# Optimization experiments

Hardware: AMD Instinct MI355X
Metric: run time of the kernel (lower is better)

Reference implementation:

```python
import jax, jax.numpy as jnp
import numpy as np

N_NODES = 100000
N_EDGES = 1600000
HID = 128
BOND = 16
BN_EPS = 1e-5


def setup_inputs() -> dict:
    key = jax.random.key(0)
    ks = jax.random.split(key, 12)
    sb = 1.0 / np.sqrt(BOND)
    sh = 1.0 / np.sqrt(HID)
    return {
        "features": jax.random.normal(ks[0], (N_NODES, HID), jnp.float32),
        "edge_feats": jax.random.normal(ks[1], (N_EDGES, BOND), jnp.float32),
        "src": jax.random.randint(ks[2], (N_EDGES,), 0, N_NODES, jnp.int32),
        "dst": jax.random.randint(ks[3], (N_EDGES,), 0, N_NODES, jnp.int32),
        "Wb": jax.random.uniform(ks[4], (HID, BOND), jnp.float32, -sb, sb),
        "bb": jax.random.uniform(ks[5], (HID,), jnp.float32, -sb, sb),
        "W1": jax.random.uniform(ks[6], (HID, HID), jnp.float32, -sh, sh),
        "b1": jax.random.uniform(ks[7], (HID,), jnp.float32, -sh, sh),
        "W2": jax.random.uniform(ks[8], (HID, HID), jnp.float32, -sh, sh),
        "b2": jax.random.uniform(ks[9], (HID,), jnp.float32, -sh, sh),
        "gamma1": jnp.ones((HID,), jnp.float32),
        "beta1": jnp.zeros((HID,), jnp.float32),
        "gamma2": jnp.ones((HID,), jnp.float32),
        "beta2": jnp.zeros((HID,), jnp.float32),
    }


def _batchnorm(x, gamma, beta):
    # BatchNorm1d in training mode: normalize with batch stats (biased var).
    mean = jnp.mean(x, axis=0)
    var = jnp.var(x, axis=0)
    return (x - mean) * jax.lax.rsqrt(var + BN_EPS) * gamma + beta


def reference(features, edge_feats, src, dst, Wb, bb, W1, b1, W2, b2,
              gamma1, beta1, gamma2, beta2):
    n = features.shape[0]
    # edge linear: [E, BOND] -> [E, HID]
    eh = edge_feats @ Wb.T + bb
    # mailbox sums: sum of src node features and edge messages per dst node
    h1 = jax.ops.segment_sum(features[src], dst, num_segments=n)  # [N, HID]
    h2 = jax.ops.segment_sum(eh, dst, num_segments=n)             # [N, HID]
    h = jax.nn.relu(_batchnorm(h1 @ W1.T + b1 + h2, gamma1, beta1))
    h = jax.nn.relu(_batchnorm(h @ W2.T + b2 + features, gamma2, beta2))
    return h
```

## Files before the change

kernel.cpp:

```cpp
#include <hip/hip_runtime.h>

#define NN 100000
#define NE 1600000
#define HID 128
#define KEXT 160
#define ROWB 320
#define BSH 9
#define BNODES 512
#define NB 196
#define P2B 256
#define EPB2 6250
#define T2 2048
#define SCAP 10240
#define BN_EPS 1e-5f

typedef __attribute__((ext_vector_type(8))) short bf16x8;
typedef __attribute__((ext_vector_type(4))) float f32x4;

__device__ inline unsigned short f2bf(float x) {
  union { float f; unsigned u; } v; v.f = x;
  unsigned r = v.u + 0x7FFFu + ((v.u >> 16) & 1u);
  return (unsigned short)(r >> 16);
}
__device__ inline unsigned pk2(float a, float b) {
  return (unsigned)f2bf(a) | ((unsigned)f2bf(b) << 16);
}
__device__ inline float bflo(unsigned p) { return __uint_as_float(p << 16); }
__device__ inline float bfhi(unsigned p) { return __uint_as_float(p & 0xffff0000u); }

__device__ inline void gload_lds16(const void* g, void* l) {
  __builtin_amdgcn_global_load_lds((const __attribute__((address_space(1))) void*)g,
                                   (__attribute__((address_space(3))) void*)l, 16, 0, 0);
}

__global__ __launch_bounds__(256) void fbw_k(const float* __restrict__ f,
                                             unsigned* __restrict__ fb,
                                             const float* __restrict__ W1,
                                             const float* __restrict__ Wb,
                                             const float* __restrict__ bb,
                                             const float* __restrict__ b1,
                                             const float* __restrict__ W2,
                                             unsigned short* __restrict__ W1e,
                                             unsigned short* __restrict__ W2e,
                                             const int* __restrict__ dst,
                                             int* __restrict__ cnts_s) {
  __shared__ int bh[NB];
  if (blockIdx.x < 25000) {
    int i = blockIdx.x * 256 + threadIdx.x;
    float2 v = ((const float2*)f)[i];
    fb[i] = pk2(v.x, v.y);
  } else if (blockIdx.x < 25080) {
    int idx = (blockIdx.x - 25000) * 256 + threadIdx.x;
    if (idx < 128 * KEXT) {
      int c = idx / KEXT, k = idx - c * KEXT;
      float v1 = 0.f;
      if (k < 128) v1 = W1[c * HID + k];
      else if (k < 144) v1 = Wb[c * 16 + (k - 128)];
      else if (k == 144) v1 = bb[c];
      else if (k == 145) v1 = b1[c];
      W1e[idx] = f2bf(v1);
    }
    if (idx < 128 * 128) W2e[idx] = f2bf(W2[(idx >> 7) * HID + (idx & 127)]);
  } else {
    int blk = blockIdx.x - 25080;
    int b0 = blk * EPB2, e1 = b0 + EPB2;
    for (int i = threadIdx.x; i < NB; i += 256) bh[i] = 0;
    __syncthreads();
    for (int e = b0 + threadIdx.x; e < e1; e += 256) atomicAdd(&bh[dst[e] >> BSH], 1);
    __syncthreads();
    for (int i = threadIdx.x; i < NB; i += 256) cnts_s[i * P2B + blk] = bh[i];
  }
}

__global__ __launch_bounds__(P2B) void cscan_k(int* __restrict__ cnts_s,
                                               int* __restrict__ bcnt_s,
                                               int* __restrict__ bcnt_r) {
  __shared__ int s[P2B];
  int b = blockIdx.x, t = threadIdx.x;
  int x = cnts_s[b * P2B + t];
  int xs = (x + 7) & ~7;
  s[t] = xs; __syncthreads();
  for (int off = 1; off < P2B; off <<= 1) {
    int v = (t >= off) ? s[t - off] : 0; __syncthreads();
    s[t] += v; __syncthreads();
  }
  cnts_s[b * P2B + t] = s[t] - xs;
  if (t == P2B - 1) bcnt_s[b] = s[t];
  __syncthreads();
  s[t] = x; __syncthreads();
  for (int off = 1; off < P2B; off <<= 1) {
    int v = (t >= off) ? s[t - off] : 0; __syncthreads();
    s[t] += v; __syncthreads();
  }
  if (t == P2B - 1) bcnt_r[b] = s[t];
}

__global__ __launch_bounds__(256) void bscan_k(const int* __restrict__ bcnt_r,
                                               const int* __restrict__ bcnt_s,
                                               int* __restrict__ bbase_r,
                                               int* __restrict__ bbase_s,
                                               int* __restrict__ rs) {
  __shared__ int s[256];
  int t = threadIdx.x;
#pragma unroll
  for (int pass = 0; pass < 2; ++pass) {
    const int* in = (pass == 0) ? bcnt_r : bcnt_s;
    int* out = (pass == 0) ? bbase_r : bbase_s;
    int x = (t < NB) ? in[t] : 0;
    s[t] = x; __syncthreads();
    for (int off = 1; off < 256; off <<= 1) {
      int v = (t >= off) ? s[t - off] : 0; __syncthreads();
      s[t] += v; __syncthreads();
    }
    if (t < NB) out[t] = s[t] - x;
    if (t == NB - 1) out[NB] = s[t];
    __syncthreads();
  }
  if (t == 0) rs[NN] = NE;
}

__global__ __launch_bounds__(1024) void part3_k(const int* __restrict__ src,
                                                const int* __restrict__ dst,
                                                const float* __restrict__ ef,
                                                const int* __restrict__ bbase_s,
                                                const int* __restrict__ cnts_s,
                                                unsigned* __restrict__ stg,
                                                float4* __restrict__ efb) {
  __shared__ int th[NB], ts[NB], cnt2[NB], run[NB], st_s[NB];
  __shared__ int sscan[256];
  __shared__ unsigned spk[T2];
  __shared__ float4 eflds[T2 * 2];
  int blk = blockIdx.x, tid = threadIdx.x;
  int b0 = blk * EPB2, e1 = b0 + EPB2;
  for (int i = tid; i < NB; i += 1024) {
    run[i] = 0;
    st_s[i] = bbase_s[i] + cnts_s[i * P2B + blk];
  }
  for (int t0 = b0; t0 < e1; t0 += T2) {
    int tc = min(T2, e1 - t0);
    for (int i = tid; i < NB; i += 1024) { th[i] = 0; cnt2[i] = 0; }
    __syncthreads();
    for (int le = tid; le < tc; le += 1024) {
      int e = t0 + le;
      atomicAdd(&th[dst[e] >> BSH], 1);
      const float4* efp = (const float4*)(ef + (size_t)e * 16);
      float4 e0 = efp[0], e1v = efp[1], e2 = efp[2], e3 = efp[3];
      float4 w0, w1;
      w0.x = __uint_as_float(pk2(e0.x, e0.y));  w0.y = __uint_as_float(pk2(e0.z, e0.w));
      w0.z = __uint_as_float(pk2(e1v.x, e1v.y)); w0.w = __uint_as_float(pk2(e1v.z, e1v.w));
      w1.x = __uint_as_float(pk2(e2.x, e2.y));  w1.y = __uint_as_float(pk2(e2.z, e2.w));
      w1.z = __uint_as_float(pk2(e3.x, e3.y));  w1.w = __uint_as_float(pk2(e3.z, e3.w));
      eflds[le * 2] = w0;
      eflds[le * 2 + 1] = w1;
    }
    __syncthreads();
    if (tid < 256) sscan[tid] = (tid < NB) ? th[tid] : 0;
    __syncthreads();
    for (int off = 1; off < 256; off <<= 1) {
      int v = 0;
      if (tid < 256 && tid >= off) v = sscan[tid - off];
      __syncthreads();
      if (tid < 256) sscan[tid] += v;
      __syncthreads();
    }
    if (tid < NB) ts[tid] = sscan[tid] - th[tid];
    __syncthreads();
    for (int le = tid; le < tc; le += 1024) {
      int b = dst[t0 + le] >> BSH;
      int slot = ts[b] + atomicAdd(&cnt2[b], 1);
      spk[slot] = ((unsigned)b << 11) | (unsigned)le;
    }
    __syncthreads();
    for (int s2 = tid; s2 < tc; s2 += 1024) {
      unsigned pk = spk[s2];
      int b = pk >> 11, le = pk & 2047;
      int e = t0 + le;
      int gs = st_s[b] + run[b] + (s2 - ts[b]);
      int d9 = dst[e] & (BNODES - 1);
      stg[gs] = (unsigned)src[e] | ((unsigned)d9 << 17) | (1u << 26);
      efb[(size_t)gs * 2] = eflds[le * 2];
      efb[(size_t)gs * 2 + 1] = eflds[le * 2 + 1];
    }
    __syncthreads();
    for (int i = tid; i < NB; i += 1024) run[i] += th[i];
    __syncthreads();
  }
  for (int i = tid; i < NB; i += 1024) {
    int c = run[i];
    int cs = (c + 7) & ~7;
    for (int j = c; j < cs; ++j) stg[st_s[i] + j] = 0u;
  }
}

__global__ __launch_bounds__(512) void bsort_k(const unsigned* __restrict__ stg,
                                               const int* __restrict__ bbase_s,
                                               const int* __restrict__ bbase_r,
                                               const unsigned* __restrict__ efbu,
                                               int* __restrict__ rs,
                                               unsigned* __restrict__ fin,
                                               unsigned* __restrict__ efsum) {
  __shared__ int h[BNODES], sc[BNODES], cur[BNODES];
  __shared__ int tot;
  __shared__ unsigned slds[SCAP];
  int b = blockIdx.x, n0 = b << BSH, tid = threadIdx.x;
  int s0p = bbase_s[b], e1p = bbase_s[b + 1];
  int s0r = bbase_r[b];
  h[tid] = 0;
  __syncthreads();
  for (int i = s0p + tid; i < e1p; i += 512) {
    unsigned rec = stg[i];
    if (rec >> 26) atomicAdd(&h[(rec >> 17) & (BNODES - 1)], 1);
  }
  __syncthreads();
  sc[tid] = h[tid];
  __syncthreads();
  for (int off = 1; off < BNODES; off <<= 1) {
    int v = (tid >= off) ? sc[tid - off] : 0;
    __syncthreads();
    sc[tid] += v;
    __syncthreads();
  }
  int excl = sc[tid] - h[tid];
  cur[tid] = excl;
  int n = n0 + tid;
  if (n < NN) rs[n] = s0r + excl;
  if (tid == BNODES - 1) tot = sc[tid];
  __syncthreads();
  for (int i = s0p + tid; i < e1p; i += 512) {
    unsigned rec = stg[i];
    if (rec >> 26) {
      int d = (rec >> 17) & (BNODES - 1);
      int p = atomicAdd(&cur[d], 1);
      slds[p] = (rec & 0x1FFFF) | ((unsigned)(i - s0p) << 17);
    }
  }
  __syncthreads();
  int T = tot;
  for (int j = tid; j < T; j += 512) fin[s0r + j] = slds[j] & 0x1FFFF;
  if (n < NN) {
    float a[16];
#pragma unroll
    for (int k = 0; k < 16; ++k) a[k] = 0.f;
    for (int j = excl; j < sc[tid]; ++j) {
      unsigned rec = slds[j];
      const unsigned* ep = efbu + ((size_t)s0p + (rec >> 17)) * 8;
#pragma unroll
      for (int k = 0; k < 8; ++k) {
        unsigned u = ep[k];
        a[2 * k] += bflo(u);
        a[2 * k + 1] += bfhi(u);
      }
    }
    unsigned* op = efsum + (size_t)n * 8;
#pragma unroll
    for (int k = 0; k < 8; ++k) op[k] = pk2(a[2 * k], a[2 * k + 1]);
  }
}

__global__ __launch_bounds__(256) void feg_k(const unsigned* __restrict__ fb,
                                             const int* __restrict__ rs,
                                             const unsigned* __restrict__ fin,
                                             const unsigned* __restrict__ efsum,
                                             unsigned short* __restrict__ A1) {
  int bid = (int)(blockIdx.x & 7) * 3125 + (int)(blockIdx.x >> 3);
  int wid = threadIdx.x >> 6, lane = threadIdx.x & 63;
  int node = bid * 4 + wid;
  if (node >= NN) return;
  int start = rs[node], end = rs[node + 1];
  float ax0 = 0.f, ay0 = 0.f, ax1 = 0.f, ay1 = 0.f;
  float ax2 = 0.f, ay2 = 0.f, ax3 = 0.f, ay3 = 0.f;
  float ax4 = 0.f, ay4 = 0.f, ax5 = 0.f, ay5 = 0.f;
  float ax6 = 0.f, ay6 = 0.f, ax7 = 0.f, ay7 = 0.f;
  int i = start;
  for (; i + 8 <= end; i += 8) {
    int sl = 0;
    if (lane < 8) sl = (int)fin[i + lane];
    int s0 = __shfl(sl, 0), s1 = __shfl(sl, 1), s2 = __shfl(sl, 2), s3 = __shfl(sl, 3);
    int s4 = __shfl(sl, 4), s5 = __shfl(sl, 5), s6 = __shfl(sl, 6), s7 = __shfl(sl, 7);
    unsigned p0 = fb[s0 * 64 + lane];
    unsigned p1 = fb[s1 * 64 + lane];
    unsigned p2 = fb[s2 * 64 + lane];
    unsigned p3 = fb[s3 * 64 + lane];
    unsigned p4 = fb[s4 * 64 + lane];
    unsigned p5 = fb[s5 * 64 + lane];
    unsigned p6 = fb[s6 * 64 + lane];
    unsigned p7 = fb[s7 * 64 + lane];
    ax0 += bflo(p0); ay0 += bfhi(p0);
    ax1 += bflo(p1); ay1 += bfhi(p1);
    ax2 += bflo(p2); ay2 += bfhi(p2);
    ax3 += bflo(p3); ay3 += bfhi(p3);
    ax4 += bflo(p4); ay4 += bfhi(p4);
    ax5 += bflo(p5); ay5 += bfhi(p5);
    ax6 += bflo(p6); ay6 += bfhi(p6);
    ax7 += bflo(p7); ay7 += bfhi(p7);
  }
  for (; i < end; ++i) {
    int sl = 0;
    if (lane == 0) sl = (int)fin[i];
    int s0 = __shfl(sl, 0);
    unsigned p0 = fb[s0 * 64 + lane];
    ax0 += bflo(p0); ay0 += bfhi(p0);
  }
  float ax = ((ax0 + ax1) + (ax2 + ax3)) + ((ax4 + ax5) + (ax6 + ax7));
  float ay = ((ay0 + ay1) + (ay2 + ay3)) + ((ay4 + ay5) + (ay6 + ay7));
  char* rowp = (char*)A1 + (size_t)node * ROWB;
  *(unsigned*)(rowp + lane * 4) = pk2(ax, ay);
  if (lane < 8) {
    *(unsigned*)(rowp + 256 + 4 * lane) = efsum[(size_t)node * 8 + lane];
  } else if (lane < 16) {
    int j2 = lane - 8;
    *(unsigned*)(rowp + 288 + 4 * j2) =
        (j2 == 0) ? pk2((float)(end - start), 1.0f) : 0u;
  }
}

__global__ __launch_bounds__(256) void gemm1_k(
    const unsigned short* __restrict__ A, const unsigned short* __restrict__ W,
    unsigned short* __restrict__ outb, float* __restrict__ ssum, float* __restrict__ ssq) {
  __shared__ __align__(16) char sA[64 * ROWB];
  __shared__ __align__(16) char sW[128 * ROWB];
  const int tid = threadIdx.x;
  const int wid = tid >> 6, lane = tid & 63;
  const size_t r0 = (size_t)blockIdx.x * 64;

#pragma unroll
  for (int q = 0; q < 5; ++q) {
    int s = q * 256 + tid;
    int row = (s * 3277) >> 16;
    int c = s - row * 20;
    int csrc = (c < 16) ? (c ^ (row & 7)) : (16 + ((c - 16) ^ (row & 3)));
    gload_lds16((const char*)A + (r0 + row) * ROWB + csrc * 16,
                sA + (size_t)(q * 256 + wid * 64) * 16);
  }
#pragma unroll
  for (int q = 0; q < 10; ++q) {
    int s = q * 256 + tid;
    int row = (s * 3277) >> 16;
    int c = s - row * 20;
    int csrc = (c < 16) ? (c ^ (row & 7)) : (16 + ((c - 16) ^ (row & 3)));
    gload_lds16((const char*)W + (size_t)row * ROWB + csrc * 16,
                sW + (size_t)(q * 256 + wid * 64) * 16);
  }
  __syncthreads();

  const int l15 = lane & 15;
  const int kgr = lane >> 4;
  const int arow = wid * 16 + l15;
  bf16x8 afrag[5];
#pragma unroll
  for (int ks = 0; ks < 5; ++ks) {
    int creq = ks * 4 + kgr;
    int csw = (creq < 16) ? (creq ^ (arow & 7)) : (16 + ((creq - 16) ^ (arow & 3)));
    afrag[ks] = *(const bf16x8*)(sA + arow * ROWB + csw * 16);
  }
  f32x4 acc[8];
#pragma unroll
  for (int ct = 0; ct < 8; ++ct) acc[ct] = (f32x4){0.f, 0.f, 0.f, 0.f};
#pragma unroll
  for (int ct = 0; ct < 8; ++ct) {
    int brow = ct * 16 + l15;
#pragma unroll
    for (int ks = 0; ks < 5; ++ks) {
      int creq = ks * 4 + kgr;
      int csw = (creq < 16) ? (creq ^ (brow & 7)) : (16 + ((creq - 16) ^ (brow & 3)));
      bf16x8 bfrag = *(const bf16x8*)(sW + brow * ROWB + csw * 16);
      acc[ct] = __builtin_amdgcn_mfma_f32_16x16x32_bf16(afrag[ks], bfrag, acc[ct], 0, 0, 0);
    }
  }

  const size_t orow0 = r0 + wid * 16 + kgr * 4;
  float cs[8], cq[8];
#pragma unroll
  for (int ct = 0; ct < 8; ++ct) {
    int col = ct * 16 + l15;
    float s_ = 0.f, q_ = 0.f;
#pragma unroll
    for (int r = 0; r < 4; ++r) {
      size_t row = orow0 + r;
      if (row < NN) {
        float v = acc[ct][r];
        outb[row * HID + col] = f2bf(v);
        s_ += v; q_ += v * v;
      }
    }
    cs[ct] = s_; cq[ct] = q_;
  }
#pragma unroll
  for (int ct = 0; ct < 8; ++ct) {
    cs[ct] += __shfl_xor(cs[ct], 16); cs[ct] += __shfl_xor(cs[ct], 32);
    cq[ct] += __shfl_xor(cq[ct], 16); cq[ct] += __shfl_xor(cq[ct], 32);
  }
  __syncthreads();
  float* red = (float*)sA;
  if (lane < 16) {
#pragma unroll
    for (int ct = 0; ct < 8; ++ct) {
      red[wid * 256 + ct * 16 + l15] = cs[ct];
      red[wid * 256 + 128 + ct * 16 + l15] = cq[ct];
    }
  }
  __syncthreads();
  if (tid < 128) {
    float s_ = red[tid] + red[256 + tid] + red[512 + tid] + red[768 + tid];
    float q_ = red[128 + tid] + red[384 + tid] + red[640 + tid] + red[896 + tid];
    atomicAdd(&ssum[tid], s_);
    atomicAdd(&ssq[tid], q_);
  }
}

__global__ __launch_bounds__(256) void gemm2_k(
    const unsigned* __restrict__ t, const unsigned short* __restrict__ W,
    const float* __restrict__ ssum, const float* __restrict__ ssq,
    const float* __restrict__ gamma, const float* __restrict__ beta,
    const float* __restrict__ b2, const float* __restrict__ F,
    unsigned short* __restrict__ outb, float* __restrict__ ssum2,
    float* __restrict__ ssq2) {
  __shared__ __align__(16) char sA[64 * 256];
  __shared__ __align__(16) char sW[128 * 256];
  __shared__ float ssc[128], ssh[128];
  const int tid = threadIdx.x;
  const int wid = tid >> 6, lane = tid & 63;
  const size_t r0 = (size_t)blockIdx.x * 64;

  if (tid < 128) {
    const float invN = 1.f / (float)NN;
    float m = ssum[tid] * invN;
    float var = ssq[tid] * invN - m * m;
    float inv = rsqrtf(var + BN_EPS);
    float sc = gamma[tid] * inv;
    ssc[tid] = sc;
    ssh[tid] = beta[tid] - m * sc;
  }
#pragma unroll
  for (int q = 0; q < 8; ++q) {
    int s = q * 256 + tid;
    int row = s >> 4, c = s & 15;
    int csrc = c ^ (row & 7);
    gload_lds16((const char*)W + (size_t)row * 256 + csrc * 16,
                sW + (size_t)(q * 256 + wid * 64) * 16);
  }
  __syncthreads();

  {
    int sr = tid >> 2;
    int c0 = (tid & 3) * 4;
    size_t grow = r0 + sr;
    bool valid = grow < NN;
    const unsigned* trow = t + grow * 64;
#pragma unroll
    for (int cc = 0; cc < 4; ++cc) {
      int c = c0 + cc;
      unsigned o0 = 0, o1 = 0, o2 = 0, o3 = 0;
      if (valid) {
        unsigned p0 = trow[c * 4 + 0], p1 = trow[c * 4 + 1];
        unsigned p2 = trow[c * 4 + 2], p3 = trow[c * 4 + 3];
        int k = c * 8;
        o0 = pk2(fmaxf(0.f, fmaf(bflo(p0), ssc[k + 0], ssh[k + 0])),
                 fmaxf(0.f, fmaf(bfhi(p0), ssc[k + 1], ssh[k + 1])));
        o1 = pk2(fmaxf(0.f, fmaf(bflo(p1), ssc[k + 2], ssh[k + 2])),
                 fmaxf(0.f, fmaf(bfhi(p1), ssc[k + 3], ssh[k + 3])));
        o2 = pk2(fmaxf(0.f, fmaf(bflo(p2), ssc[k + 4], ssh[k + 4])),
                 fmaxf(0.f, fmaf(bfhi(p2), ssc[k + 5], ssh[k + 5])));
        o3 = pk2(fmaxf(0.f, fmaf(bflo(p3), ssc[k + 6], ssh[k + 6])),
                 fmaxf(0.f, fmaf(bfhi(p3), ssc[k + 7], ssh[k + 7])));
      }
      int csw = c ^ (sr & 7);
      uint4 w4; w4.x = o0; w4.y = o1; w4.z = o2; w4.w = o3;
      *(uint4*)(sA + sr * 256 + csw * 16) = w4;
    }
  }
  __syncthreads();

  const int l15 = lane & 15;
  const int kgr = lane >> 4;
  const int arow = wid * 16 + l15;
  bf16x8 afrag[4];
#pragma unroll
  for (int ks = 0; ks < 4; ++ks) {
    int creq = ks * 4 + kgr;
    int csw = creq ^ (arow & 7);
    afrag[ks] = *(const bf16x8*)(sA + arow * 256 + csw * 16);
  }
  f32x4 acc[8];
#pragma unroll
  for (int ct = 0; ct < 8; ++ct) acc[ct] = (f32x4){0.f, 0.f, 0.f, 0.f};
#pragma unroll
  for (int ct = 0; ct < 8; ++ct) {
    int brow = ct * 16 + l15;
#pragma unroll
    for (int ks = 0; ks < 4; ++ks) {
      int creq = ks * 4 + kgr;
      int csw = creq ^ (brow & 7);
      bf16x8 bfrag = *(const bf16x8*)(sW + brow * 256 + csw * 16);
      acc[ct] = __builtin_amdgcn_mfma_f32_16x16x32_bf16(afrag[ks], bfrag, acc[ct], 0, 0, 0);
    }
  }

  const size_t orow0 = r0 + wid * 16 + kgr * 4;
  float cs[8], cq[8];
#pragma unroll
  for (int ct = 0; ct < 8; ++ct) {
    int col = ct * 16 + l15;
    float b2v = b2[col];
    float s_ = 0.f, q_ = 0.f;
#pragma unroll
    for (int r = 0; r < 4; ++r) {
      size_t row = orow0 + r;
      if (row < NN) {
        float v = acc[ct][r] + b2v + F[row * HID + col];
        outb[row * HID + col] = f2bf(v);
        s_ += v; q_ += v * v;
      }
    }
    cs[ct] = s_; cq[ct] = q_;
  }
#pragma unroll
  for (int ct = 0; ct < 8; ++ct) {
    cs[ct] += __shfl_xor(cs[ct], 16); cs[ct] += __shfl_xor(cs[ct], 32);
    cq[ct] += __shfl_xor(cq[ct], 16); cq[ct] += __shfl_xor(cq[ct], 32);
  }
  __syncthreads();
  float* red = (float*)sA;
  if (lane < 16) {
#pragma unroll
    for (int ct = 0; ct < 8; ++ct) {
      red[wid * 256 + ct * 16 + l15] = cs[ct];
      red[wid * 256 + 128 + ct * 16 + l15] = cq[ct];
    }
  }
  __syncthreads();
  if (tid < 128) {
    float s_ = red[tid] + red[256 + tid] + red[512 + tid] + red[768 + tid];
    float q_ = red[128 + tid] + red[384 + tid] + red[640 + tid] + red[896 + tid];
    atomicAdd(&ssum2[tid], s_);
    atomicAdd(&ssq2[tid], q_);
  }
}

__global__ __launch_bounds__(256) void bn_final_k(const unsigned* __restrict__ t,
                                                  const float* __restrict__ ssum,
                                                  const float* __restrict__ ssq,
                                                  const float* __restrict__ gamma,
                                                  const float* __restrict__ beta,
                                                  float* __restrict__ o) {
  __shared__ float ssc[128], ssh[128];
  int tid = threadIdx.x;
  if (tid < 128) {
    const float invN = 1.f / (float)NN;
    float m = ssum[tid] * invN;
    float var = ssq[tid] * invN - m * m;
    float inv = rsqrtf(var + BN_EPS);
    float sc = gamma[tid] * inv;
    ssc[tid] = sc;
    ssh[tid] = beta[tid] - m * sc;
  }
  __syncthreads();
  int i = blockIdx.x * 256 + tid;
  if (i >= NN * 64) return;
  unsigned p = t[i];
  int c = (i & 63) * 2;
  float2 v;
  v.x = fmaxf(0.f, fmaf(bflo(p), ssc[c], ssh[c]));
  v.y = fmaxf(0.f, fmaf(bfhi(p), ssc[c + 1], ssh[c + 1]));
  ((float2*)o)[i] = v;
}

extern "C" void kernel_launch(void* const* d_in, const int* in_sizes, int n_in,
                              void* d_out, int out_size, void* d_ws, size_t ws_size,
                              hipStream_t stream) {
  (void)in_sizes; (void)n_in; (void)out_size; (void)ws_size;
  const float* features   = (const float*)d_in[0];
  const float* edge_feats = (const float*)d_in[1];
  const int*   src        = (const int*)d_in[2];
  const int*   dst        = (const int*)d_in[3];
  const float* Wb         = (const float*)d_in[4];
  const float* bb         = (const float*)d_in[5];
  const float* W1         = (const float*)d_in[6];
  const float* b1         = (const float*)d_in[7];
  const float* W2         = (const float*)d_in[8];
  const float* b2         = (const float*)d_in[9];
  const float* gamma1     = (const float*)d_in[10];
  const float* beta1      = (const float*)d_in[11];
  const float* gamma2     = (const float*)d_in[12];
  const float* beta2      = (const float*)d_in[13];
  float* outp = (float*)d_out;

  char* wsb = (char*)d_ws;
  size_t off = 0;
  auto alloc = [&](size_t nbytes) -> void* {
    off = (off + 255) & ~(size_t)255;
    void* p = wsb + off;
    off += nbytes;
    return p;
  };
  const size_t STGN = (size_t)NE + 7 * NB * P2B + 64;
  int* row_start = (int*)alloc((size_t)(NN + 1) * 4);
  int* bcnt_r    = (int*)alloc(NB * 4);
  int* bcnt_s    = (int*)alloc(NB * 4);
  int* bbase_r   = (int*)alloc((NB + 1) * 4);
  int* bbase_s   = (int*)alloc((NB + 1) * 4);
  int* cnts_s    = (int*)alloc((size_t)NB * P2B * 4);
  float* stats   = (float*)alloc(512 * 4);
  unsigned* featb = (unsigned*)alloc((size_t)NN * 64 * 4);
  unsigned short* A1e = (unsigned short*)alloc((size_t)100032 * ROWB);
  unsigned short* W1e = (unsigned short*)alloc(128 * KEXT * 2);
  unsigned short* W2e = (unsigned short*)alloc(128 * 128 * 2);
  unsigned* stg  = (unsigned*)alloc(STGN * 4);
  unsigned* fin  = (unsigned*)alloc((size_t)NE * 4);
  float4* efb    = (float4*)alloc(STGN * 32);
  unsigned* efsum = (unsigned*)alloc((size_t)NN * 32);
  unsigned short* tbuf = (unsigned short*)featb;

  hipMemsetAsync(stats, 0, 512 * 4, stream);
  hipMemsetAsync((char*)A1e + (size_t)NN * ROWB, 0, 32 * ROWB, stream);

  fbw_k<<<25336, 256, 0, stream>>>(features, featb, W1, Wb, bb, b1, W2, W1e, W2e,
                                   dst, cnts_s);
  cscan_k<<<NB, P2B, 0, stream>>>(cnts_s, bcnt_s, bcnt_r);
  bscan_k<<<1, 256, 0, stream>>>(bcnt_r, bcnt_s, bbase_r, bbase_s, row_start);
  part3_k<<<P2B, 1024, 0, stream>>>(src, dst, edge_feats, bbase_s, cnts_s, stg, efb);
  bsort_k<<<NB, 512, 0, stream>>>(stg, bbase_s, bbase_r, (const unsigned*)efb,
                                  row_start, fin, efsum);
  feg_k<<<25000, 256, 0, stream>>>(featb, row_start, fin, efsum, A1e);

  gemm1_k<<<1563, 256, 0, stream>>>(A1e, W1e, tbuf, stats, stats + 128);
  gemm2_k<<<1563, 256, 0, stream>>>((const unsigned*)tbuf, W2e, stats, stats + 128,
                                    gamma1, beta1, b2, features, tbuf,
                                    stats + 256, stats + 384);
  bn_final_k<<<25000, 256, 0, stream>>>((const unsigned*)tbuf, stats + 256, stats + 384,
                                        gamma2, beta2, outp);
}
```

Measured before the change: 333.0 us.

## Double GEMM row tiles to 128 and shard BN stat atomics across 16 slots

Both GEMM kernels now process 128 rows per block, using two 16-row MFMA tiles per wave that share each B fragment load, and the grid is halved. BatchNorm statistics are accumulated into 16 partial slots indexed by block to reduce atomic contention. Small single-block kernels reduce those slots and precompute scale/shift, so the per-block BN setup in gemm2 and bn_final is removed. gemm2's A staging now uses vectorized uint4 loads, and the padded buffers are zeroed so the larger tiles can read past NN safely. In exchange there are two extra tiny launches and more LDS and registers per block, which may lower occupancy.

Result: faster. 304.1 us (-8.7%).

```diff
diff --git a/kernel.cpp b/kernel.cpp
--- a/kernel.cpp
+++ b/kernel.cpp
@@ -12,6 +12,8 @@
 #define EPB2 6250
 #define T2 2048
 #define SCAP 10240
+#define NROWP 100096
+#define GGRID 782
 #define BN_EPS 1e-5f
 
 typedef __attribute__((ext_vector_type(8))) short bf16x8;
@@ -316,15 +318,15 @@
 
 __global__ __launch_bounds__(256) void gemm1_k(
     const unsigned short* __restrict__ A, const unsigned short* __restrict__ W,
-    unsigned short* __restrict__ outb, float* __restrict__ ssum, float* __restrict__ ssq) {
-  __shared__ __align__(16) char sA[64 * ROWB];
+    unsigned short* __restrict__ outb, float* __restrict__ statsP) {
+  __shared__ __align__(16) char sA[128 * ROWB];
   __shared__ __align__(16) char sW[128 * ROWB];
   const int tid = threadIdx.x;
   const int wid = tid >> 6, lane = tid & 63;
-  const size_t r0 = (size_t)blockIdx.x * 64;
-
-#pragma unroll
-  for (int q = 0; q < 5; ++q) {
+  const size_t r0 = (size_t)blockIdx.x * 128;
+
+#pragma unroll
+  for (int q = 0; q < 10; ++q) {
     int s = q * 256 + tid;
     int row = (s * 3277) >> 16;
     int c = s - row * 20;
@@ -345,17 +347,22 @@
 
   const int l15 = lane & 15;
   const int kgr = lane >> 4;
-  const int arow = wid * 16 + l15;
-  bf16x8 afrag[5];
-#pragma unroll
-  for (int ks = 0; ks < 5; ++ks) {
-    int creq = ks * 4 + kgr;
-    int csw = (creq < 16) ? (creq ^ (arow & 7)) : (16 + ((creq - 16) ^ (arow & 3)));
-    afrag[ks] = *(const bf16x8*)(sA + arow * ROWB + csw * 16);
-  }
-  f32x4 acc[8];
-#pragma unroll
-  for (int ct = 0; ct < 8; ++ct) acc[ct] = (f32x4){0.f, 0.f, 0.f, 0.f};
+  bf16x8 afrag[2][5];
+#pragma unroll
+  for (int rt = 0; rt < 2; ++rt) {
+    int arow = wid * 32 + rt * 16 + l15;
+#pragma unroll
+    for (int ks = 0; ks < 5; ++ks) {
+      int creq = ks * 4 + kgr;
+      int csw = (creq < 16) ? (creq ^ (arow & 7)) : (16 + ((creq - 16) ^ (arow & 3)));
+      afrag[rt][ks] = *(const bf16x8*)(sA + arow * ROWB + csw * 16);
+    }
+  }
+  f32x4 acc[2][8];
+#pragma unroll
+  for (int rt = 0; rt < 2; ++rt)
+#pragma unroll
+    for (int ct = 0; ct < 8; ++ct) acc[rt][ct] = (f32x4){0.f, 0.f, 0.f, 0.f};
 #pragma unroll
   for (int ct = 0; ct < 8; ++ct) {
     int brow = ct * 16 + l15;
@@ -364,26 +371,30 @@
       int creq = ks * 4 + kgr;
       int csw = (creq < 16) ? (creq ^ (brow & 7)) : (16 + ((creq - 16) ^ (brow & 3)));
       bf16x8 bfrag = *(const bf16x8*)(sW + brow * ROWB + csw * 16);
-      acc[ct] = __builtin_amdgcn_mfma_f32_16x16x32_bf16(afrag[ks], bfrag, acc[ct], 0, 0, 0);
-    }
-  }
-
-  const size_t orow0 = r0 + wid * 16 + kgr * 4;
+      acc[0][ct] = __builtin_amdgcn_mfma_f32_16x16x32_bf16(afrag[0][ks], bfrag, acc[0][ct], 0, 0, 0);
+      acc[1][ct] = __builtin_amdgcn_mfma_f32_16x16x32_bf16(afrag[1][ks], bfrag, acc[1][ct], 0, 0, 0);
+    }
+  }
+
   float cs[8], cq[8];
 #pragma unroll
-  for (int ct = 0; ct < 8; ++ct) {
-    int col = ct * 16 + l15;
-    float s_ = 0.f, q_ = 0.f;
-#pragma unroll
-    for (int r = 0; r < 4; ++r) {
-      size_t row = orow0 + r;
-      if (row < NN) {
-        float v = acc[ct][r];
-        outb[row * HID + col] = f2bf(v);
-        s_ += v; q_ += v * v;
+  for (int ct = 0; ct < 8; ++ct) { cs[ct] = 0.f; cq[ct] = 0.f; }
+#pragma unroll
+  for (int rt = 0; rt < 2; ++rt) {
+    const size_t orow0 = r0 + wid * 32 + rt * 16 + kgr * 4;
+#pragma unroll
+    for (int ct = 0; ct < 8; ++ct) {
+      int col = ct * 16 + l15;
+#pragma unroll
+      for (int r = 0; r < 4; ++r) {
+        size_t row = orow0 + r;
+        if (row < NN) {
+          float v = acc[rt][ct][r];
+          outb[row * HID + col] = f2bf(v);
+          cs[ct] += v; cq[ct] += v * v;
+        }
       }
     }
-    cs[ct] = s_; cq[ct] = q_;
   }
 #pragma unroll
   for (int ct = 0; ct < 8; ++ct) {
@@ -400,36 +411,49 @@
     }
   }
   __syncthreads();
-  if (tid < 128) {
+  if (tid < 256) {
+    float* base = statsP + (size_t)(blockIdx.x & 15) * 512;
     float s_ = red[tid] + red[256 + tid] + red[512 + tid] + red[768 + tid];
-    float q_ = red[128 + tid] + red[384 + tid] + red[640 + tid] + red[896 + tid];
-    atomicAdd(&ssum[tid], s_);
-    atomicAdd(&ssq[tid], q_);
+    atomicAdd(&base[tid], s_);
+  }
+}
+
+__global__ void bnred_k(const float* __restrict__ statsP, int base,
+                        const float* __restrict__ gamma, const float* __restrict__ beta,
+                        float* __restrict__ scale, float* __restrict__ shift) {
+  int c = threadIdx.x;
+  if (c < 128) {
+    float s_ = 0.f, q_ = 0.f;
+#pragma unroll
+    for (int i = 0; i < 16; ++i) {
+      s_ += statsP[i * 512 + base + c];
+      q_ += statsP[i * 512 + base + 128 + c];
+    }
+    const float invN = 1.f / (float)NN;
+    float m = s_ * invN;
+    float var = q_ * invN - m * m;
+    float inv = rsqrtf(var + BN_EPS);
+    float sc = gamma[c] * inv;
+    scale[c] = sc;
+    shift[c] = beta[c] - m * sc;
   }
 }
 
 __global__ __launch_bounds__(256) void gemm2_k(
     const unsigned* __restrict__ t, const unsigned short* __restrict__ W,
-    const float* __restrict__ ssum, const float* __restrict__ ssq,
-    const float* __restrict__ gamma, const float* __restrict__ beta,
+    const float* __restrict__ scale, const float* __restrict__ shift,
     const float* __restrict__ b2, const float* __restrict__ F,
-    unsigned short* __restrict__ outb, float* __restrict__ ssum2,
-    float* __restrict__ ssq2) {
-  __shared__ __align__(16) char sA[64 * 256];
+    unsigned short* __restrict__ outb, float* __restrict__ statsP) {
+  __shared__ __align__(16) char sA[128 * 256];
   __shared__ __align__(16) char sW[128 * 256];
   __shared__ float ssc[128], ssh[128];
   const int tid = threadIdx.x;
   const int wid = tid >> 6, lane = tid & 63;
-  const size_t r0 = (size_t)blockIdx.x * 64;
+  const size_t r0 = (size_t)blockIdx.x * 128;
 
   if (tid < 128) {
-    const float invN = 1.f / (float)NN;
-    float m = ssum[tid] * invN;
-    float var = ssq[tid] * invN - m * m;
-    float inv = rsqrtf(var + BN_EPS);
-    float sc = gamma[tid] * inv;
-    ssc[tid] = sc;
-    ssh[tid] = beta[tid] - m * sc;
+    ssc[tid] = scale[tid];
+    ssh[tid] = shift[tid];
   }
 #pragma unroll
   for (int q = 0; q < 8; ++q) {
@@ -441,49 +465,46 @@
   }
   __syncthreads();
 
-  {
-    int sr = tid >> 2;
-    int c0 = (tid & 3) * 4;
+#pragma unroll
+  for (int q = 0; q < 8; ++q) {
+    int s = q * 256 + tid;
+    int sr = s >> 4, c = s & 15;
     size_t grow = r0 + sr;
-    bool valid = grow < NN;
-    const unsigned* trow = t + grow * 64;
-#pragma unroll
-    for (int cc = 0; cc < 4; ++cc) {
-      int c = c0 + cc;
-      unsigned o0 = 0, o1 = 0, o2 = 0, o3 = 0;
-      if (valid) {
-        unsigned p0 = trow[c * 4 + 0], p1 = trow[c * 4 + 1];
-        unsigned p2 = trow[c * 4 + 2], p3 = trow[c * 4 + 3];
-        int k = c * 8;
-        o0 = pk2(fmaxf(0.f, fmaf(bflo(p0), ssc[k + 0], ssh[k + 0])),
-                 fmaxf(0.f, fmaf(bfhi(p0), ssc[k + 1], ssh[k + 1])));
-        o1 = pk2(fmaxf(0.f, fmaf(bflo(p1), ssc[k + 2], ssh[k + 2])),
-                 fmaxf(0.f, fmaf(bfhi(p1), ssc[k + 3], ssh[k + 3])));
-        o2 = pk2(fmaxf(0.f, fmaf(bflo(p2), ssc[k + 4], ssh[k + 4])),
-                 fmaxf(0.f, fmaf(bfhi(p2), ssc[k + 5], ssh[k + 5])));
-        o3 = pk2(fmaxf(0.f, fmaf(bflo(p3), ssc[k + 6], ssh[k + 6])),
-                 fmaxf(0.f, fmaf(bfhi(p3), ssc[k + 7], ssh[k + 7])));
-      }
-      int csw = c ^ (sr & 7);
-      uint4 w4; w4.x = o0; w4.y = o1; w4.z = o2; w4.w = o3;
-      *(uint4*)(sA + sr * 256 + csw * 16) = w4;
-    }
+    uint4 v = make_uint4(0, 0, 0, 0);
+    if (grow < NN) v = *(const uint4*)(t + grow * 64 + c * 4);
+    int k = c * 8;
+    unsigned o0 = pk2(fmaxf(0.f, fmaf(bflo(v.x), ssc[k + 0], ssh[k + 0])),
+                      fmaxf(0.f, fmaf(bfhi(v.x), ssc[k + 1], ssh[k + 1])));
+    unsigned o1 = pk2(fmaxf(0.f, fmaf(bflo(v.y), ssc[k + 2], ssh[k + 2])),
+                      fmaxf(0.f, fmaf(bfhi(v.y), ssc[k + 3], ssh[k + 3])));
+    unsigned o2 = pk2(fmaxf(0.f, fmaf(bflo(v.z), ssc[k + 4], ssh[k + 4])),
+                      fmaxf(0.f, fmaf(bfhi(v.z), ssc[k + 5], ssh[k + 5])));
+    unsigned o3 = pk2(fmaxf(0.f, fmaf(bflo(v.w), ssc[k + 6], ssh[k + 6])),
+                      fmaxf(0.f, fmaf(bfhi(v.w), ssc[k + 7], ssh[k + 7])));
+    int csw = c ^ (sr & 7);
+    uint4 w4; w4.x = o0; w4.y = o1; w4.z = o2; w4.w = o3;
+    *(uint4*)(sA + sr * 256 + csw * 16) = w4;
   }
   __syncthreads();
 
   const int l15 = lane & 15;
   const int kgr = lane >> 4;
-  const int arow = wid * 16 + l15;
-  bf16x8 afrag[4];
-#pragma unroll
-  for (int ks = 0; ks < 4; ++ks) {
-    int creq = ks * 4 + kgr;
-    int csw = creq ^ (arow & 7);
-    afrag[ks] = *(const bf16x8*)(sA + arow * 256 + csw * 16);
-  }
-  f32x4 acc[8];
-#pragma unroll
-  for (int ct = 0; ct < 8; ++ct) acc[ct] = (f32x4){0.f, 0.f, 0.f, 0.f};
+  bf16x8 afrag[2][4];
+#pragma unroll
+  for (int rt = 0; rt < 2; ++rt) {
+    int arow = wid * 32 + rt * 16 + l15;
+#pragma unroll
+    for (int ks = 0; ks < 4; ++ks) {
+      int creq = ks * 4 + kgr;
+      int csw = creq ^ (arow & 7);
+      afrag[rt][ks] = *(const bf16x8*)(sA + arow * 256 + csw * 16);
+    }
+  }
+  f32x4 acc[2][8];
+#pragma unroll
+  for (int rt = 0; rt < 2; ++rt)
+#pragma unroll
+    for (int ct = 0; ct < 8; ++ct) acc[rt][ct] = (f32x4){0.f, 0.f, 0.f, 0.f};
 #pragma unroll
   for (int ct = 0; ct < 8; ++ct) {
     int brow = ct * 16 + l15;
@@ -492,27 +513,31 @@
       int creq = ks * 4 + kgr;
       int csw = creq ^ (brow & 7);
       bf16x8 bfrag = *(const bf16x8*)(sW + brow * 256 + csw * 16);
-      acc[ct] = __builtin_amdgcn_mfma_f32_16x16x32_bf16(afrag[ks], bfrag, acc[ct], 0, 0, 0);
-    }
-  }
-
-  const size_t orow0 = r0 + wid * 16 + kgr * 4;
+      acc[0][ct] = __builtin_amdgcn_mfma_f32_16x16x32_bf16(afrag[0][ks], bfrag, acc[0][ct], 0, 0, 0);
+      acc[1][ct] = __builtin_amdgcn_mfma_f32_16x16x32_bf16(afrag[1][ks], bfrag, acc[1][ct], 0, 0, 0);
+    }
+  }
+
   float cs[8], cq[8];
 #pragma unroll
-  for (int ct = 0; ct < 8; ++ct) {
-    int col = ct * 16 + l15;
-    float b2v = b2[col];
-    float s_ = 0.f, q_ = 0.f;
-#pragma unroll
-    for (int r = 0; r < 4; ++r) {
-      size_t row = orow0 + r;
-      if (row < NN) {
-        float v = acc[ct][r] + b2v + F[row * HID + col];
-        outb[row * HID + col] = f2bf(v);
-        s_ += v; q_ += v * v;
+  for (int ct = 0; ct < 8; ++ct) { cs[ct] = 0.f; cq[ct] = 0.f; }
+#pragma unroll
+  for (int rt = 0; rt < 2; ++rt) {
+    const size_t orow0 = r0 + wid * 32 + rt * 16 + kgr * 4;
+#pragma unroll
+    for (int ct = 0; ct < 8; ++ct) {
+      int col = ct * 16 + l15;
+      float b2v = b2[col];
+#pragma unroll
+      for (int r = 0; r < 4; ++r) {
+        size_t row = orow0 + r;
+        if (row < NN) {
+          float v = acc[rt][ct][r] + b2v + F[row * HID + col];
+          outb[row * HID + col] = f2bf(v);
+          cs[ct] += v; cq[ct] += v * v;
+        }
       }
     }
-    cs[ct] = s_; cq[ct] = q_;
   }
 #pragma unroll
   for (int ct = 0; ct < 8; ++ct) {
@@ -529,31 +554,20 @@
     }
   }
   __syncthreads();
-  if (tid < 128) {
+  if (tid < 256) {
+    float* base = statsP + (size_t)(blockIdx.x & 15) * 512 + 256;
     float s_ = red[tid] + red[256 + tid] + red[512 + tid] + red[768 + tid];
-    float q_ = red[128 + tid] + red[384 + tid] + red[640 + tid] + red[896 + tid];
-    atomicAdd(&ssum2[tid], s_);
-    atomicAdd(&ssq2[tid], q_);
+    atomicAdd(&base[tid], s_);
   }
 }
 
 __global__ __launch_bounds__(256) void bn_final_k(const unsigned* __restrict__ t,
-                                                  const float* __restrict__ ssum,
-                                                  const float* __restrict__ ssq,
-                                                  const float* __restrict__ gamma,
-                                                  const float* __restrict__ beta,
+                                                  const float* __restrict__ scale,
+                                                  const float* __restrict__ shift,
                                                   float* __restrict__ o) {
   __shared__ float ssc[128], ssh[128];
   int tid = threadIdx.x;
-  if (tid < 128) {
-    const float invN = 1.f / (float)NN;
-    float m = ssum[tid] * invN;
-    float var = ssq[tid] * invN - m * m;
-    float inv = rsqrtf(var + BN_EPS);
-    float sc = gamma[tid] * inv;
-    ssc[tid] = sc;
-    ssh[tid] = beta[tid] - m * sc;
-  }
+  if (tid < 128) { ssc[tid] = scale[tid]; ssh[tid] = shift[tid]; }
   __syncthreads();
   int i = blockIdx.x * 256 + tid;
   if (i >= NN * 64) return;
@@ -600,9 +614,10 @@
   int* bbase_r   = (int*)alloc((NB + 1) * 4);
   int* bbase_s   = (int*)alloc((NB + 1) * 4);
   int* cnts_s    = (int*)alloc((size_t)NB * P2B * 4);
-  float* stats   = (float*)alloc(512 * 4);
-  unsigned* featb = (unsigned*)alloc((size_t)NN * 64 * 4);
-  unsigned short* A1e = (unsigned short*)alloc((size_t)100032 * ROWB);
+  float* statsP  = (float*)alloc(16 * 512 * 4);
+  float* scsh    = (float*)alloc(512 * 4);
+  unsigned* featb = (unsigned*)alloc((size_t)NROWP * 64 * 4);
+  unsigned short* A1e = (unsigned short*)alloc((size_t)NROWP * ROWB);
   unsigned short* W1e = (unsigned short*)alloc(128 * KEXT * 2);
   unsigned short* W2e = (unsigned short*)alloc(128 * 128 * 2);
   unsigned* stg  = (unsigned*)alloc(STGN * 4);
@@ -611,8 +626,9 @@
   unsigned* efsum = (unsigned*)alloc((size_t)NN * 32);
   unsigned short* tbuf = (unsigned short*)featb;
 
-  hipMemsetAsync(stats, 0, 512 * 4, stream);
-  hipMemsetAsync((char*)A1e + (size_t)NN * ROWB, 0, 32 * ROWB, stream);
+  hipMemsetAsync(statsP, 0, 16 * 512 * 4, stream);
+  hipMemsetAsync((char*)A1e + (size_t)NN * ROWB, 0, (NROWP - NN) * ROWB, stream);
+  hipMemsetAsync((char*)featb + (size_t)NN * 256, 0, (NROWP - NN) * 256, stream);
 
   fbw_k<<<25336, 256, 0, stream>>>(features, featb, W1, Wb, bb, b1, W2, W1e, W2e,
                                    dst, cnts_s);
@@ -623,10 +639,11 @@
                                   row_start, fin, efsum);
   feg_k<<<25000, 256, 0, stream>>>(featb, row_start, fin, efsum, A1e);
 
-  gemm1_k<<<1563, 256, 0, stream>>>(A1e, W1e, tbuf, stats, stats + 128);
-  gemm2_k<<<1563, 256, 0, stream>>>((const unsigned*)tbuf, W2e, stats, stats + 128,
-                                    gamma1, beta1, b2, features, tbuf,
-                                    stats + 256, stats + 384);
-  bn_final_k<<<25000, 256, 0, stream>>>((const unsigned*)tbuf, stats + 256, stats + 384,
-                                        gamma2, beta2, outp);
-}
+  gemm1_k<<<GGRID, 256, 0, stream>>>(A1e, W1e, tbuf, statsP);
+  bnred_k<<<1, 128, 0, stream>>>(statsP, 0, gamma1, beta1, scsh, scsh + 128);
+  gemm2_k<<<GGRID, 256, 0, stream>>>((const unsigned*)tbuf, W2e, scsh, scsh + 128,
+                                     b2, features, tbuf, statsP);
+  bnred_k<<<1, 128, 0, stream>>>(statsP, 256, gamma2, beta2, scsh + 256, scsh + 384);
+  bn_final_k<<<25000, 256, 0, stream>>>((const unsigned*)tbuf, scsh + 256, scsh + 384,
+                                        outp);
+}
```
